# Kernel tuning notes

Measured on AMD Instinct MI355X. Metric: run time of the kernel, lower is better.

Reference implementation:

```python
import jax, jax.numpy as jnp
import numpy as np

STD = 1.0

def setup_inputs() -> dict:
    key = jax.random.key(0)
    k1, k2, k3 = jax.random.split(key, 3)
    B, G, D = 16384, 8192, 64
    return {
        "input": jax.random.normal(k1, (B, D), dtype=jnp.float32),
        "inputs": jax.random.normal(k2, (G, D), dtype=jnp.float32),
        "weights": jax.random.normal(k3, (G,), dtype=jnp.float32),
    }

def reference(input, inputs, weights):
    dot_prod = jnp.einsum("bd,gd->bg", input, inputs)
    norm_input = jnp.sum(input * input, axis=-1, keepdims=True)   # [B, 1]
    norm_inputs = jnp.sum(inputs * inputs, axis=-1)               # [G]
    distance = norm_input + norm_inputs - 2.0 * dot_prod          # [B, G]
    # Gaussian kernel weighted sum over centers -> [B]
    out = jnp.einsum("bg,g->b", jnp.exp(-distance / (2.0 * STD * STD)), weights)
    return out
```

## Files before the change

### kernel.cpp

```cpp
#include <hip/hip_runtime.h>


typedef __attribute__((ext_vector_type(8))) _Float16 half8v;
typedef __attribute__((ext_vector_type(16))) float f32x16;
typedef unsigned short u16;
typedef unsigned int u32;

#define L2E   1.4426950408889634f
#define NHL2E 0.72134752044448170f
#define GSPLIT 8

#define MFMA(a,b,c) __builtin_amdgcn_mfma_f32_32x32x16_f16(a,b,c,0,0,0)

__global__ __launch_bounds__(256)
void convert_C(const float* __restrict__ C, const float* __restrict__ W,
               _Float16* __restrict__ Cf, float2* __restrict__ cw, int G){
  int idx = blockIdx.x*256 + threadIdx.x;
  int g = idx >> 2, f = idx & 3;
  if (g >= G) return;
  const float* row = C + (size_t)g*64 + f*16;
  int cg = g >> 5, cl = g & 31;
  float norm = 0.f;
  _Float16 hv[16];
  #pragma unroll
  for (int q=0; q<4; q++){
    float4 v = *(const float4*)(row + q*4);
    float xv[4] = {v.x, v.y, v.z, v.w};
    #pragma unroll
    for (int e=0; e<4; e++){
      float x = xv[e];
      norm = fmaf(x, x, norm);
      hv[q*4+e] = (_Float16)x;
    }
  }
  norm += __shfl_xor(norm, 1);
  norm += __shfl_xor(norm, 2);
  size_t u = ((size_t)(cg*4 + f)*64 + cl)*8;
  *(half8v*)(Cf + u)       = *(half8v*)hv;
  *(half8v*)(Cf + u + 256) = *(half8v*)(hv + 8);
  if (f == 0) cw[g] = make_float2(-NHL2E*norm, W[g]);
}

__global__ __launch_bounds__(256, 2)
void rbf_mfma(const float* __restrict__ X, const _Float16* __restrict__ Cf,
              const float2* __restrict__ cw, float* __restrict__ out){
  const int tid = threadIdx.x;
  const int l  = tid & 63;
  const int cl = l & 31;
  const int h  = l >> 5;
  const int w  = tid >> 6;
  const int b  = blockIdx.x;
  const int gp = b & 7;
  const int rows0 = ((b >> 3)*4 + w) * 64;

  half8v af[2][4];
  float xn[2];
  #pragma unroll
  for (int rf=0; rf<2; rf++){
    const float* xr = X + (size_t)(rows0 + rf*32 + cl)*64;
    float s = 0.f;
    #pragma unroll
    for (int f=0; f<4; f++){
      float4 v0 = *(const float4*)(xr + f*16 + h*8);
      float4 v1 = *(const float4*)(xr + f*16 + h*8 + 4);
      float xv[8] = {v0.x,v0.y,v0.z,v0.w,v1.x,v1.y,v1.z,v1.w};
      _Float16 hv[8];
      #pragma unroll
      for (int e=0;e<8;e++){
        float x = xv[e];
        s = fmaf(x, x, s);
        hv[e] = (_Float16)x;
      }
      af[rf][f] = *(half8v*)hv;
    }
    s += __shfl_xor(s, 32);
    xn[rf] = -NHL2E * s;
  }

  const char* baseF = (const char*)Cf + (size_t)gp*131072 + (size_t)l*16;
  const float2* cwp = cw + gp*1024 + cl;

  half8v bf[2];
  bf[0] = *(const half8v*)baseF;

  float racc0[16], racc1[16];
  #pragma unroll
  for (int r=0;r<16;r++){ racc0[r]=0.f; racc1[r]=0.f; }

  f32x16 aE0, aE1, aO0, aO1;
  float2 cwE, cwO;

  #define EPIX(P, R, CWV, RACC)                                             \
    RACC[R] = fmaf(__builtin_amdgcn_exp2f(fmaf(P[R], L2E, CWV.x)),          \
                   CWV.y, RACC[R])

  #define TILE(T, C0, C1, P0, P1, CWC, CWP, DO_EPI) do {                    \
    const int t_ = (T);                                                     \
    CWC = cwp[t_*32];                                                       \
    C0 = (f32x16){}; C1 = (f32x16){};                                       \
    _Pragma("unroll")                                                       \
    for (int f=0; f<4; ++f){                                                \
      const int p = f & 1, q = p ^ 1;                                       \
      const int nf = (f + 1) & 3;                                           \
      const int nt = (f == 3) ? ((t_ + 1) & 31) : t_;                       \
      bf[q] = *(const half8v*)(baseF + (size_t)nt*4096 + (size_t)nf*1024);  \
      C0 = MFMA(af[0][f], bf[p], C0);                                       \
      if (DO_EPI){                                                          \
        EPIX(P0, f*4+0, CWP, racc0); EPIX(P1, f*4+0, CWP, racc1);           \
        EPIX(P0, f*4+1, CWP, racc0); EPIX(P1, f*4+1, CWP, racc1);           \
      }                                                                     \
      C1 = MFMA(af[1][f], bf[p], C1);                                       \
      if (DO_EPI){                                                          \
        EPIX(P0, f*4+2, CWP, racc0); EPIX(P1, f*4+2, CWP, racc1);           \
        EPIX(P0, f*4+3, CWP, racc0); EPIX(P1, f*4+3, CWP, racc1);           \
      }                                                                     \
    }                                                                       \
  } while(0)

  TILE(0, aE0, aE1, aO0, aO1, cwE, cwO, 0);
  #pragma unroll 1
  for (int tp = 0; tp < 15; ++tp){
    TILE(2*tp + 1, aO0, aO1, aE0, aE1, cwO, cwE, 1);
    TILE(2*tp + 2, aE0, aE1, aO0, aO1, cwE, cwO, 1);
  }
  TILE(31, aO0, aO1, aE0, aE1, cwO, cwE, 1);
  #pragma unroll
  for (int r=0;r<16;++r){
    EPIX(aO0, r, cwO, racc0);
    EPIX(aO1, r, cwO, racc1);
  }
  #undef TILE
  #undef EPIX

  #pragma unroll
  for (int rf=0; rf<2; rf++){
    #pragma unroll
    for (int r=0;r<16;r++){
      float v = rf ? racc1[r] : racc0[r];
      v += __shfl_xor(v, 1);
      v += __shfl_xor(v, 2);
      v += __shfl_xor(v, 4);
      v += __shfl_xor(v, 8);
      v += __shfl_xor(v, 16);
      const int rit = (r&3) + 8*(r>>2) + 4*h;
      const float xnv = __shfl(xn[rf], rit);
      if (cl == 0)
        atomicAdd(&out[rows0 + rf*32 + rit], v * __builtin_amdgcn_exp2f(xnv));
    }
  }
}

extern "C" void kernel_launch(void* const* d_in, const int* in_sizes, int n_in,
                              void* d_out, int out_size, void* d_ws, size_t ws_size,
                              hipStream_t stream) {
  const float* X = (const float*)d_in[0];
  const float* C = (const float*)d_in[1];
  const float* W = (const float*)d_in[2];
  float* out = (float*)d_out;
  const int B = in_sizes[0] / 64;
  const int G = in_sizes[2];

  _Float16* Cf = (_Float16*)d_ws;
  float2* cw = (float2*)(Cf + (size_t)G*64);

  hipMemsetAsync(out, 0, (size_t)B*sizeof(float), stream);
  convert_C<<<(G*4)/256, 256, 0, stream>>>(C, W, Cf, cw, G);
  rbf_mfma<<<(B/256)*GSPLIT, 256, 0, stream>>>(X, Cf, cw, out);
}
```

Measured before the change: 48.55 us.

## Stage center tiles in LDS via async global-to-LDS loads and split G into 16

```diff
diff --git a/kernel.cpp b/kernel.cpp
--- a/kernel.cpp
+++ b/kernel.cpp
@@ -8,9 +8,14 @@
 
 #define L2E   1.4426950408889634f
 #define NHL2E 0.72134752044448170f
-#define GSPLIT 8
+#define GP 16
 
 #define MFMA(a,b,c) __builtin_amdgcn_mfma_f32_32x32x16_f16(a,b,c,0,0,0)
+
+__device__ __forceinline__ void gl_lds16(const void* g, void* l){
+  __builtin_amdgcn_global_load_lds((const __attribute__((address_space(1))) u32*)g,
+                                   (__attribute__((address_space(3))) u32*)l, 16, 0, 0);
+}
 
 __global__ __launch_bounds__(256)
 void convert_C(const float* __restrict__ C, const float* __restrict__ W,
@@ -44,14 +49,33 @@
 __global__ __launch_bounds__(256, 2)
 void rbf_mfma(const float* __restrict__ X, const _Float16* __restrict__ Cf,
               const float2* __restrict__ cw, float* __restrict__ out){
+  __shared__ __align__(16) half8v Bs[16*4*64];
+  __shared__ __align__(16) float2 cwsh[512];
+
   const int tid = threadIdx.x;
   const int l  = tid & 63;
   const int cl = l & 31;
   const int h  = l >> 5;
   const int w  = tid >> 6;
   const int b  = blockIdx.x;
-  const int gp = b & 7;
-  const int rows0 = ((b >> 3)*4 + w) * 64;
+  const int gp = b & 15;
+  const int rows0 = (b >> 4) * 256 + w * 64;
+
+  {
+    const char* src = (const char*)Cf + (size_t)(gp*16)*4096 + (size_t)l*16;
+    char* dst = (char*)Bs;
+    #pragma unroll
+    for (int j=0; j<4; ++j){
+      const int tt = w*4 + j;
+      #pragma unroll
+      for (int f=0; f<4; ++f){
+        const size_t o = (size_t)(tt*4 + f)*1024;
+        gl_lds16(src + o, dst + o);
+      }
+    }
+    gl_lds16((const char*)(cw + gp*512) + (size_t)w*1024 + (size_t)l*16,
+             (char*)cwsh + (size_t)w*1024);
+  }
 
   half8v af[2][4];
   float xn[2];
@@ -77,11 +101,11 @@
     xn[rf] = -NHL2E * s;
   }
 
-  const char* baseF = (const char*)Cf + (size_t)gp*131072 + (size_t)l*16;
-  const float2* cwp = cw + gp*1024 + cl;
+  asm volatile("s_waitcnt vmcnt(0)" ::: "memory");
+  __syncthreads();
 
   half8v bf[2];
-  bf[0] = *(const half8v*)baseF;
+  bf[0] = Bs[l];
 
   float racc0[16], racc1[16];
   #pragma unroll
@@ -96,14 +120,14 @@
 
   #define TILE(T, C0, C1, P0, P1, CWC, CWP, DO_EPI) do {                    \
     const int t_ = (T);                                                     \
-    CWC = cwp[t_*32];                                                       \
+    CWC = cwsh[t_*32 + cl];                                                 \
     C0 = (f32x16){}; C1 = (f32x16){};                                       \
     _Pragma("unroll")                                                       \
     for (int f=0; f<4; ++f){                                                \
       const int p = f & 1, q = p ^ 1;                                       \
       const int nf = (f + 1) & 3;                                           \
-      const int nt = (f == 3) ? ((t_ + 1) & 31) : t_;                       \
-      bf[q] = *(const half8v*)(baseF + (size_t)nt*4096 + (size_t)nf*1024);  \
+      const int nt = (f == 3) ? ((t_ + 1) & 15) : t_;                       \
+      bf[q] = Bs[(nt*4 + nf)*64 + l];                                       \
       C0 = MFMA(af[0][f], bf[p], C0);                                       \
       if (DO_EPI){                                                          \
         EPIX(P0, f*4+0, CWP, racc0); EPIX(P1, f*4+0, CWP, racc1);           \
@@ -119,11 +143,11 @@
 
   TILE(0, aE0, aE1, aO0, aO1, cwE, cwO, 0);
   #pragma unroll 1
-  for (int tp = 0; tp < 15; ++tp){
+  for (int tp = 0; tp < 7; ++tp){
     TILE(2*tp + 1, aO0, aO1, aE0, aE1, cwO, cwE, 1);
     TILE(2*tp + 2, aE0, aE1, aO0, aO1, cwE, cwO, 1);
   }
-  TILE(31, aO0, aO1, aE0, aE1, cwO, cwE, 1);
+  TILE(15, aO0, aO1, aE0, aE1, cwO, cwE, 1);
   #pragma unroll
   for (int r=0;r<16;++r){
     EPIX(aO0, r, cwO, racc0);
@@ -165,5 +189,5 @@
 
   hipMemsetAsync(out, 0, (size_t)B*sizeof(float), stream);
   convert_C<<<(G*4)/256, 256, 0, stream>>>(C, W, Cf, cw, G);
-  rbf_mfma<<<(B/256)*GSPLIT, 256, 0, stream>>>(X, Cf, cw, out);
+  rbf_mfma<<<(B/256)*GP, 256, 0, stream>>>(X, Cf, cw, out);
 }
```

Result: no change. 48.70 us (+0.3%).
